# Kernel tuning notes

Measured on AMD Instinct MI355X. Metric: run time of the kernel, lower is better.

Reference implementation:

```python
import jax, jax.numpy as jnp
import numpy as np

B, IN_F, OUT_F = 4096, 4096, 11008  # tokens, in_features, out_features


def setup_inputs() -> dict:
    key = jax.random.key(0)
    k1, k2, k3, k4 = jax.random.split(key, 4)
    x = jax.random.normal(k1, (B, IN_F), dtype=jnp.float32)
    # Each int holds two packed 4-bit codes (low nibble = even col, high nibble = odd col).
    packed_weights = jax.random.randint(k2, (OUT_F, IN_F // 2), 0, 256, dtype=jnp.int32)
    scales = jax.random.uniform(k3, (OUT_F,), dtype=jnp.float32) * 0.02 + 1e-4
    zero_points = jax.random.uniform(k4, (OUT_F,), dtype=jnp.float32) * 15.0
    return {"x": x, "packed_weights": packed_weights, "scales": scales,
            "zero_points": zero_points}


def _dequantize(packed_weights, scales, zero_points):
    # Unpack two 4-bit codes per byte -> q: [OUT_F, IN_F]
    low = (packed_weights & 15).astype(jnp.float32)
    high = ((packed_weights >> 4) & 15).astype(jnp.float32)
    q = jnp.stack([low, high], axis=-1).reshape(packed_weights.shape[0], -1)
    # Per-row affine dequant: w = (q - zero_point) * scale
    return (q - zero_points[:, None]) * scales[:, None]


def reference(x, packed_weights, scales, zero_points):
    W = _dequantize(packed_weights, scales, zero_points)  # [OUT_F, IN_F]
    return x @ W.T  # [B, OUT_F]
```

## Files before the change

### kernel.cpp

```cpp
#include <hip/hip_runtime.h>
#include <hip/hip_bf16.h>
#include <stdint.h>

#define M_DIM 4096
#define N_DIM 11008
#define K_DIM 4096
#define KP    (K_DIM / 2)

typedef __attribute__((ext_vector_type(4))) int i32x4;

#define AS1 __attribute__((address_space(1)))
#define AS3 __attribute__((address_space(3)))

__global__ __launch_bounds__(256) void prep(const float* __restrict__ x,
                                            const int* __restrict__ pw,
                                            signed char* __restrict__ xq,
                                            signed char* __restrict__ wq,
                                            float* __restrict__ r,
                                            float* __restrict__ sx) {
  const int b = blockIdx.x;
  const int t = threadIdx.x;
  if (b < 4096) {
    const int row = b;
    const int lane = t & 63, wid = t >> 6;
    const float4* x4 = (const float4*)(x + (size_t)row * K_DIM);
    float4 v[4];
    float am = 0.0f, sm = 0.0f;
#pragma unroll
    for (int i = 0; i < 4; ++i) {
      v[i] = x4[i * 256 + t];
      sm += v[i].x + v[i].y + v[i].z + v[i].w;
      am = fmaxf(am, fmaxf(fmaxf(fabsf(v[i].x), fabsf(v[i].y)),
                           fmaxf(fabsf(v[i].z), fabsf(v[i].w))));
    }
#pragma unroll
    for (int off = 32; off >= 1; off >>= 1) {
      am = fmaxf(am, __shfl_xor(am, off));
      sm += __shfl_xor(sm, off);
    }
    __shared__ float smax[4], ssum[4];
    if (lane == 0) { smax[wid] = am; ssum[wid] = sm; }
    __syncthreads();
    am = fmaxf(fmaxf(smax[0], smax[1]), fmaxf(smax[2], smax[3]));
    sm = ssum[0] + ssum[1] + ssum[2] + ssum[3];
    const float inv = am > 0.0f ? 127.0f / am : 0.0f;
    unsigned int* xo = (unsigned int*)(xq + (size_t)row * K_DIM);
#pragma unroll
    for (int i = 0; i < 4; ++i) {
      int q0 = min(127, max(-127, __float2int_rn(v[i].x * inv)));
      int q1 = min(127, max(-127, __float2int_rn(v[i].y * inv)));
      int q2 = min(127, max(-127, __float2int_rn(v[i].z * inv)));
      int q3 = min(127, max(-127, __float2int_rn(v[i].w * inv)));
      xo[i * 256 + t] = ((unsigned int)q0 & 0xFF) | (((unsigned int)q1 & 0xFF) << 8) |
                        (((unsigned int)q2 & 0xFF) << 16) | (((unsigned int)q3 & 0xFF) << 24);
    }
    if (t == 0) { r[row] = sm; sx[row] = am > 0.0f ? am / 127.0f : 0.0f; }
  } else {
    const int total = (N_DIM * KP) / 4;
    for (int i = (b - 4096) * 256 + t; i < total; i += 2048 * 256) {
      int4 p = ((const int4*)pw)[i];
      int v[4] = {p.x, p.y, p.z, p.w};
      unsigned int u0 = 0, u1 = 0;
#pragma unroll
      for (int j = 0; j < 2; ++j) {
        unsigned int b0 = (unsigned int)(2 * (v[j] & 15) - 15) & 0xFF;
        unsigned int b1 = (unsigned int)(2 * ((v[j] >> 4) & 15) - 15) & 0xFF;
        u0 |= (b0 | (b1 << 8)) << (16 * j);
      }
#pragma unroll
      for (int j = 0; j < 2; ++j) {
        unsigned int b0 = (unsigned int)(2 * (v[2 + j] & 15) - 15) & 0xFF;
        unsigned int b1 = (unsigned int)(2 * ((v[2 + j] >> 4) & 15) - 15) & 0xFF;
        u1 |= (b0 | (b1 << 8)) << (16 * j);
      }
      uint2 st; st.x = u0; st.y = u1;
      ((uint2*)wq)[i] = st;
    }
  }
}

#define BM 256
#define BN 256
#define BK 128
#define NTILE (K_DIM / BK)
#define NT_M (M_DIM / BM)
#define NT_N (N_DIM / BN)
#define NWG  (NT_M * NT_N)
#define HS 16384
#define PS 65536

#define WAITV(n) asm volatile("s_waitcnt vmcnt(" #n ")" ::: "memory")
#define WAITL0   asm volatile("s_waitcnt lgkmcnt(0)" ::: "memory")
#define BARR     do { asm volatile("" ::: "memory"); __builtin_amdgcn_s_barrier(); asm volatile("" ::: "memory"); } while (0)
#define SCHED0   __builtin_amdgcn_sched_barrier(0)

__global__ __launch_bounds__(512, 2) void gemm_i8(const signed char* __restrict__ Xq,
                                                  const signed char* __restrict__ Wq,
                                                  const float* __restrict__ sc,
                                                  const float* __restrict__ zp,
                                                  const float* __restrict__ rbuf,
                                                  const float* __restrict__ sxbuf,
                                                  float* __restrict__ C) {
  __shared__ __align__(16) unsigned char lds8[131072];

  const int t = threadIdx.x;
  const int bid = blockIdx.x;
  const int swz = (bid & 7) * (NWG / 8) + (bid >> 3);
  const int tm = swz & 15;
  const int tn = swz >> 4;

  const int srow = t >> 3;
  const int g0 = (t & 7) ^ (srow & 7);
  const int koff = g0 * 16;
  const signed char* pB0c0 = Wq + (size_t)(tn * BN + srow) * K_DIM + koff;
  const signed char* pB0c1 = Wq + (size_t)(tn * BN + 64 + srow) * K_DIM + koff;
  const signed char* pB1c0 = Wq + (size_t)(tn * BN + 128 + srow) * K_DIM + koff;
  const signed char* pB1c1 = Wq + (size_t)(tn * BN + 192 + srow) * K_DIM + koff;
  const signed char* pA0c0 = Xq + (size_t)(tm * BM + srow) * K_DIM + koff;
  const signed char* pA0c1 = Xq + (size_t)(tm * BM + 64 + srow) * K_DIM + koff;
  const signed char* pA1c0 = Xq + (size_t)(tm * BM + 128 + srow) * K_DIM + koff;
  const signed char* pA1c1 = Xq + (size_t)(tm * BM + 192 + srow) * K_DIM + koff;
  const int d0 = t * 16;
  const int d1 = d0 + 8192;

  const int lane = t & 63;
  const int w = t >> 6;
  const int wm = w >> 2;
  const int wn = w & 3;
  const int lr = lane & 15, lk = lane >> 4;

  const int j0 = lk ^ (lr & 7);
  const int aB0 = (2 + wm) * HS + lr * 128 + j0 * 16;
  const int aB1 = aB0 ^ 64;
  const int bB0 = (wn >> 1) * HS + (wn & 1) * 8192 + lr * 128 + j0 * 16;
  const int bB1 = bB0 ^ 64;

  i32x4 acc[8][4] = {};

#define GLL(src, dstoff) \
  __builtin_amdgcn_global_load_lds((const AS1 void*)(src), (AS3 void*)(lds8 + (dstoff)), 16, 0, 0)

  GLL(pB0c0, 0 * HS + d0); GLL(pB0c1, 0 * HS + d1);
  GLL(pB1c0, 1 * HS + d0); GLL(pB1c1, 1 * HS + d1);
  GLL(pA0c0, 2 * HS + d0); GLL(pA0c1, 2 * HS + d1);
  GLL(pA1c0, 3 * HS + d0); GLL(pA1c1, 3 * HS + d1);
  GLL(pB0c0 + BK, 4 * HS + d0); GLL(pB0c1 + BK, 4 * HS + d1);
  GLL(pB1c0 + BK, 5 * HS + d0); GLL(pB1c1 + BK, 5 * HS + d1);
  pB0c0 += 2 * BK; pB0c1 += 2 * BK; pB1c0 += 2 * BK; pB1c1 += 2 * BK;
  pA0c0 += BK;     pA0c1 += BK;     pA1c0 += BK;     pA1c1 += BK;
  WAITV(4);
  BARR;

#define TILE(P, SA, SB, VMODE) do {                                                        \
    i32x4 a0[4], a1[4], a2[4], a3[4], b0[4], b1[4];                                        \
                  \
    _Pragma("unroll") for (int i = 0; i < 4; ++i)                                          \
      a0[i] = *(const i32x4*)(lds8 + (P) * PS + aB0 + i * 2048);                           \
    _Pragma("unroll") for (int n = 0; n < 4; ++n)                                          \
      b0[n] = *(const i32x4*)(lds8 + (P) * PS + bB0 + n * 2048);                           \
    _Pragma("unroll") for (int i = 0; i < 4; ++i)                                          \
      a1[i] = *(const i32x4*)(lds8 + (P) * PS + aB0 + (4 + i) * 2048);                     \
    if (SA) { GLL(pA0c0, (((P) ^ 1) * 4 + 2) * HS + d0);                                   \
              GLL(pA0c1, (((P) ^ 1) * 4 + 2) * HS + d1);                                   \
              pA0c0 += BK; pA0c1 += BK; }                                                  \
    SCHED0;                                                                                \
    _Pragma("unroll") for (int i = 0; i < 4; ++i)                                          \
      _Pragma("unroll") for (int n = 0; n < 4; ++n)                                        \
        acc[i][n] = __builtin_amdgcn_mfma_i32_16x16x64_i8(a0[i], b0[n], acc[i][n], 0, 0, 0); \
     \
    _Pragma("unroll") for (int n = 0; n < 4; ++n)                                          \
      b1[n] = *(const i32x4*)(lds8 + (P) * PS + bB1 + n * 2048);                           \
    _Pragma("unroll") for (int i = 0; i < 4; ++i)                                          \
      a2[i] = *(const i32x4*)(lds8 + (P) * PS + aB1 + i * 2048);                           \
    if (SA) { GLL(pA1c0, (((P) ^ 1) * 4 + 3) * HS + d0);                                   \
              GLL(pA1c1, (((P) ^ 1) * 4 + 3) * HS + d1);                                   \
              pA1c0 += BK; pA1c1 += BK; }                                                  \
    SCHED0;                                                                                \
    _Pragma("unroll") for (int i = 0; i < 4; ++i)                                          \
      _Pragma("unroll") for (int n = 0; n < 4; ++n)                                        \
        acc[4 + i][n] = __builtin_amdgcn_mfma_i32_16x16x64_i8(a1[i], b0[n], acc[4 + i][n], 0, 0, 0); \
    WAITL0;                                                                                \
    BARR;                                                                                  \
                            \
    _Pragma("unroll") for (int i = 0; i < 4; ++i)                                          \
      a3[i] = *(const i32x4*)(lds8 + (P) * PS + aB1 + (4 + i) * 2048);                     \
    if (SB) { GLL(pB0c0, ((P) * 4 + 0) * HS + d0);                                         \
              GLL(pB0c1, ((P) * 4 + 0) * HS + d1);                                         \
              pB0c0 += BK; pB0c1 += BK; }                                                  \
    SCHED0;                                                                                \
    _Pragma("unroll") for (int i = 0; i < 4; ++i)                                          \
      _Pragma("unroll") for (int n = 0; n < 4; ++n)                                        \
        acc[i][n] = __builtin_amdgcn_mfma_i32_16x16x64_i8(a2[i], b1[n], acc[i][n], 0, 0, 0); \
                        \
    if (SB) { GLL(pB1c0, ((P) * 4 + 1) * HS + d0);                                         \
              GLL(pB1c1, ((P) * 4 + 1) * HS + d1);                                         \
              pB1c0 += BK; pB1c1 += BK; }                                                  \
    SCHED0;                                                                                \
    _Pragma("unroll") for (int i = 0; i < 4; ++i)                                          \
      _Pragma("unroll") for (int n = 0; n < 4; ++n)                                        \
        acc[4 + i][n] = __builtin_amdgcn_mfma_i32_16x16x64_i8(a3[i], b1[n], acc[4 + i][n], 0, 0, 0); \
    if ((VMODE) == 0) { WAITV(4); } else if ((VMODE) == 1) { WAITV(0); }                   \
    BARR;                                                                                  \
  } while (0)

  for (int it = 0; it < (NTILE - 2) / 2; ++it) {
    TILE(0, 1, 1, 0);
    TILE(1, 1, 1, 0);
  }
  TILE(0, 1, 0, 1);
  TILE(1, 0, 0, 2);

#undef TILE
#undef GLL

  const int row0 = tm * BM + wm * 128 + lk * 4;
  const int col0 = tn * BN + wn * 64 + lr;
  float sv[4], zv[4];
#pragma unroll
  for (int n = 0; n < 4; ++n) {
    sv[n] = sc[col0 + n * 16];
    zv[n] = 7.5f - zp[col0 + n * 16];
  }
#pragma unroll
  for (int m = 0; m < 8; ++m)
#pragma unroll
    for (int rr = 0; rr < 4; ++rr) {
      const int row = row0 + m * 16 + rr;
      const float rv = rbuf[row];
      const float hx = 0.5f * sxbuf[row];
#pragma unroll
      for (int n = 0; n < 4; ++n)
        C[(size_t)row * N_DIM + col0 + n * 16] = sv[n] * (hx * (float)acc[m][n][rr] + zv[n] * rv);
    }
}

__global__ __launch_bounds__(256) void fallback_gemm(const float* __restrict__ x,
                                                     const int* __restrict__ pw,
                                                     const float* __restrict__ sc,
                                                     const float* __restrict__ zp,
                                                     float* __restrict__ out) {
  __shared__ float Xs[64][33];
  __shared__ float Ws[64][33];
  const int bid = blockIdx.x;
  const int bm = bid & 63;
  const int bn = bid >> 6;
  const int t = threadIdx.x;
  const int tx = t & 15, ty = t >> 4;
  float acc[4][4] = {};
  for (int k0 = 0; k0 < K_DIM; k0 += 32) {
    __syncthreads();
#pragma unroll
    for (int i = 0; i < 8; ++i) {
      int e = t + i * 256; int rr = e >> 5, c = e & 31;
      Xs[rr][c] = x[(size_t)(bm * 64 + rr) * K_DIM + k0 + c];
    }
#pragma unroll
    for (int i = 0; i < 4; ++i) {
      int e = t + i * 256; int rr = e >> 4, jj = e & 15;
      int row = bn * 64 + rr;
      int v = pw[(size_t)row * KP + (k0 >> 1) + jj];
      float s = sc[row], z = zp[row];
      Ws[rr][2 * jj]     = ((float)(v & 15) - z) * s;
      Ws[rr][2 * jj + 1] = ((float)((v >> 4) & 15) - z) * s;
    }
    __syncthreads();
#pragma unroll
    for (int kk = 0; kk < 32; ++kk) {
      float a[4], b[4];
#pragma unroll
      for (int i2 = 0; i2 < 4; ++i2) a[i2] = Xs[ty * 4 + i2][kk];
#pragma unroll
      for (int j2 = 0; j2 < 4; ++j2) b[j2] = Ws[tx * 4 + j2][kk];
#pragma unroll
      for (int i2 = 0; i2 < 4; ++i2)
#pragma unroll
        for (int j2 = 0; j2 < 4; ++j2) acc[i2][j2] += a[i2] * b[j2];
    }
  }
#pragma unroll
  for (int i2 = 0; i2 < 4; ++i2)
#pragma unroll
    for (int j2 = 0; j2 < 4; ++j2)
      out[(size_t)(bm * 64 + ty * 4 + i2) * N_DIM + bn * 64 + tx * 4 + j2] = acc[i2][j2];
}

extern "C" void kernel_launch(void* const* d_in, const int* in_sizes, int n_in,
                              void* d_out, int out_size, void* d_ws, size_t ws_size,
                              hipStream_t stream) {
  const float* x  = (const float*)d_in[0];
  const int*   pw = (const int*)d_in[1];
  const float* sc = (const float*)d_in[2];
  const float* zp = (const float*)d_in[3];
  float* out = (float*)d_out;

  const size_t wq_b = (size_t)N_DIM * K_DIM;
  const size_t xq_b = (size_t)M_DIM * K_DIM;
  const size_t need = wq_b + xq_b + 2 * 4096 * sizeof(float);

  if (ws_size >= need) {
    signed char* wq = (signed char*)d_ws;
    signed char* xq = wq + wq_b;
    float* rbuf  = (float*)((char*)d_ws + wq_b + xq_b);
    float* sxbuf = rbuf + 4096;
    hipLaunchKernelGGL(prep,    dim3(4096 + 2048), dim3(256), 0, stream, x, pw, xq, wq, rbuf, sxbuf);
    hipLaunchKernelGGL(gemm_i8, dim3(NWG),         dim3(512), 0, stream, xq, wq, sc, zp, rbuf, sxbuf, out);
  } else {
    hipLaunchKernelGGL(fallback_gemm, dim3(64 * 172), dim3(256), 0, stream, x, pw, sc, zp, out);
  }
}
```

Baseline: 216.8 us.

## Split GEMM workgroup into 16 waves each computing a 64x64 sub-tile

Doubles the workgroup to 1024 threads so each of 16 waves owns a 64x64 output tile instead of 128x64. Accumulator registers are halved and each thread issues one global-to-LDS load per stage instead of two. The pipeline wait counts and the epilogue row mapping are adjusted to match. The aim is more resident waves to hide latency, at the cost of more LDS reads per MFMA and tighter register limits from the new launch bounds.

```diff
diff --git a/kernel.cpp b/kernel.cpp
--- a/kernel.cpp
+++ b/kernel.cpp
@@ -94,13 +94,13 @@
 #define BARR     do { asm volatile("" ::: "memory"); __builtin_amdgcn_s_barrier(); asm volatile("" ::: "memory"); } while (0)
 #define SCHED0   __builtin_amdgcn_sched_barrier(0)
 
-__global__ __launch_bounds__(512, 2) void gemm_i8(const signed char* __restrict__ Xq,
-                                                  const signed char* __restrict__ Wq,
-                                                  const float* __restrict__ sc,
-                                                  const float* __restrict__ zp,
-                                                  const float* __restrict__ rbuf,
-                                                  const float* __restrict__ sxbuf,
-                                                  float* __restrict__ C) {
+__global__ __launch_bounds__(1024, 4) void gemm_i8(const signed char* __restrict__ Xq,
+                                                   const signed char* __restrict__ Wq,
+                                                   const float* __restrict__ sc,
+                                                   const float* __restrict__ zp,
+                                                   const float* __restrict__ rbuf,
+                                                   const float* __restrict__ sxbuf,
+                                                   float* __restrict__ C) {
   __shared__ __align__(16) unsigned char lds8[131072];
 
   const int t = threadIdx.x;
@@ -112,16 +112,11 @@
   const int srow = t >> 3;
   const int g0 = (t & 7) ^ (srow & 7);
   const int koff = g0 * 16;
-  const signed char* pB0c0 = Wq + (size_t)(tn * BN + srow) * K_DIM + koff;
-  const signed char* pB0c1 = Wq + (size_t)(tn * BN + 64 + srow) * K_DIM + koff;
-  const signed char* pB1c0 = Wq + (size_t)(tn * BN + 128 + srow) * K_DIM + koff;
-  const signed char* pB1c1 = Wq + (size_t)(tn * BN + 192 + srow) * K_DIM + koff;
-  const signed char* pA0c0 = Xq + (size_t)(tm * BM + srow) * K_DIM + koff;
-  const signed char* pA0c1 = Xq + (size_t)(tm * BM + 64 + srow) * K_DIM + koff;
-  const signed char* pA1c0 = Xq + (size_t)(tm * BM + 128 + srow) * K_DIM + koff;
-  const signed char* pA1c1 = Xq + (size_t)(tm * BM + 192 + srow) * K_DIM + koff;
-  const int d0 = t * 16;
-  const int d1 = d0 + 8192;
+  const signed char* pB0 = Wq + (size_t)(tn * BN + srow) * K_DIM + koff;
+  const signed char* pB1 = Wq + (size_t)(tn * BN + 128 + srow) * K_DIM + koff;
+  const signed char* pA0 = Xq + (size_t)(tm * BM + srow) * K_DIM + koff;
+  const signed char* pA1 = Xq + (size_t)(tm * BM + 128 + srow) * K_DIM + koff;
+  const int d = t * 16;
 
   const int lane = t & 63;
   const int w = t >> 6;
@@ -130,76 +125,57 @@
   const int lr = lane & 15, lk = lane >> 4;
 
   const int j0 = lk ^ (lr & 7);
-  const int aB0 = (2 + wm) * HS + lr * 128 + j0 * 16;
-  const int aB1 = aB0 ^ 64;
-  const int bB0 = (wn >> 1) * HS + (wn & 1) * 8192 + lr * 128 + j0 * 16;
-  const int bB1 = bB0 ^ 64;
-
-  i32x4 acc[8][4] = {};
+  const int aB0 = (2 + (wm >> 1)) * HS + ((wm & 1) * 64 + lr) * 128 + j0 * 16;
+  const int bB0 = (wn >> 1) * HS + ((wn & 1) * 64 + lr) * 128 + j0 * 16;
+
+  i32x4 acc[4][4] = {};
 
 #define GLL(src, dstoff) \
   __builtin_amdgcn_global_load_lds((const AS1 void*)(src), (AS3 void*)(lds8 + (dstoff)), 16, 0, 0)
 
-  GLL(pB0c0, 0 * HS + d0); GLL(pB0c1, 0 * HS + d1);
-  GLL(pB1c0, 1 * HS + d0); GLL(pB1c1, 1 * HS + d1);
-  GLL(pA0c0, 2 * HS + d0); GLL(pA0c1, 2 * HS + d1);
-  GLL(pA1c0, 3 * HS + d0); GLL(pA1c1, 3 * HS + d1);
-  GLL(pB0c0 + BK, 4 * HS + d0); GLL(pB0c1 + BK, 4 * HS + d1);
-  GLL(pB1c0 + BK, 5 * HS + d0); GLL(pB1c1 + BK, 5 * HS + d1);
-  pB0c0 += 2 * BK; pB0c1 += 2 * BK; pB1c0 += 2 * BK; pB1c1 += 2 * BK;
-  pA0c0 += BK;     pA0c1 += BK;     pA1c0 += BK;     pA1c1 += BK;
-  WAITV(4);
+  GLL(pB0, 0 * HS + d);
+  GLL(pB1, 1 * HS + d);
+  GLL(pA0, 2 * HS + d);
+  GLL(pA1, 3 * HS + d);
+  GLL(pB0 + BK, 4 * HS + d);
+  GLL(pB1 + BK, 5 * HS + d);
+  pB0 += 2 * BK; pB1 += 2 * BK;
+  pA0 += BK;     pA1 += BK;
+  WAITV(2);
   BARR;
 
 #define TILE(P, SA, SB, VMODE) do {                                                        \
-    i32x4 a0[4], a1[4], a2[4], a3[4], b0[4], b1[4];                                        \
-                  \
+    i32x4 a0[4], b0[4], a1[4], b1[4];                                                      \
+                            \
     _Pragma("unroll") for (int i = 0; i < 4; ++i)                                          \
       a0[i] = *(const i32x4*)(lds8 + (P) * PS + aB0 + i * 2048);                           \
     _Pragma("unroll") for (int n = 0; n < 4; ++n)                                          \
       b0[n] = *(const i32x4*)(lds8 + (P) * PS + bB0 + n * 2048);                           \
-    _Pragma("unroll") for (int i = 0; i < 4; ++i)                                          \
-      a1[i] = *(const i32x4*)(lds8 + (P) * PS + aB0 + (4 + i) * 2048);                     \
-    if (SA) { GLL(pA0c0, (((P) ^ 1) * 4 + 2) * HS + d0);                                   \
-              GLL(pA0c1, (((P) ^ 1) * 4 + 2) * HS + d1);                                   \
-              pA0c0 += BK; pA0c1 += BK; }                                                  \
+    if (SA) { GLL(pA0, (((P) ^ 1) * 4 + 2) * HS + d); pA0 += BK; }                         \
     SCHED0;                                                                                \
     _Pragma("unroll") for (int i = 0; i < 4; ++i)                                          \
       _Pragma("unroll") for (int n = 0; n < 4; ++n)                                        \
         acc[i][n] = __builtin_amdgcn_mfma_i32_16x16x64_i8(a0[i], b0[n], acc[i][n], 0, 0, 0); \
      \
+    _Pragma("unroll") for (int i = 0; i < 4; ++i)                                          \
+      a1[i] = *(const i32x4*)(lds8 + (P) * PS + (aB0 ^ 64) + i * 2048);                    \
     _Pragma("unroll") for (int n = 0; n < 4; ++n)                                          \
-      b1[n] = *(const i32x4*)(lds8 + (P) * PS + bB1 + n * 2048);                           \
-    _Pragma("unroll") for (int i = 0; i < 4; ++i)                                          \
-      a2[i] = *(const i32x4*)(lds8 + (P) * PS + aB1 + i * 2048);                           \
-    if (SA) { GLL(pA1c0, (((P) ^ 1) * 4 + 3) * HS + d0);                                   \
-              GLL(pA1c1, (((P) ^ 1) * 4 + 3) * HS + d1);                                   \
-              pA1c0 += BK; pA1c1 += BK; }                                                  \
+      b1[n] = *(const i32x4*)(lds8 + (P) * PS + (bB0 ^ 64) + n * 2048);                    \
+    if (SA) { GLL(pA1, (((P) ^ 1) * 4 + 3) * HS + d); pA1 += BK; }                         \
     SCHED0;                                                                                \
     _Pragma("unroll") for (int i = 0; i < 4; ++i)                                          \
-      _Pragma("unroll") for (int n = 0; n < 4; ++n)                                        \
-        acc[4 + i][n] = __builtin_amdgcn_mfma_i32_16x16x64_i8(a1[i], b0[n], acc[4 + i][n], 0, 0, 0); \
+      _Pragma("unroll") for (int n = 0; n < 2; ++n)                                        \
+        acc[i][n] = __builtin_amdgcn_mfma_i32_16x16x64_i8(a1[i], b1[n], acc[i][n], 0, 0, 0); \
     WAITL0;                                                                                \
     BARR;                                                                                  \
-                            \
-    _Pragma("unroll") for (int i = 0; i < 4; ++i)                                          \
-      a3[i] = *(const i32x4*)(lds8 + (P) * PS + aB1 + (4 + i) * 2048);                     \
-    if (SB) { GLL(pB0c0, ((P) * 4 + 0) * HS + d0);                                         \
-              GLL(pB0c1, ((P) * 4 + 0) * HS + d1);                                         \
-              pB0c0 += BK; pB0c1 += BK; }                                                  \
+                 \
+    if (SB) { GLL(pB0, ((P) * 4 + 0) * HS + d); pB0 += BK;                                 \
+              GLL(pB1, ((P) * 4 + 1) * HS + d); pB1 += BK; }                               \
     SCHED0;                                                                                \
     _Pragma("unroll") for (int i = 0; i < 4; ++i)                                          \
-      _Pragma("unroll") for (int n = 0; n < 4; ++n)                                        \
-        acc[i][n] = __builtin_amdgcn_mfma_i32_16x16x64_i8(a2[i], b1[n], acc[i][n], 0, 0, 0); \
-                        \
-    if (SB) { GLL(pB1c0, ((P) * 4 + 1) * HS + d0);                                         \
-              GLL(pB1c1, ((P) * 4 + 1) * HS + d1);                                         \
-              pB1c0 += BK; pB1c1 += BK; }                                                  \
-    SCHED0;                                                                                \
-    _Pragma("unroll") for (int i = 0; i < 4; ++i)                                          \
-      _Pragma("unroll") for (int n = 0; n < 4; ++n)                                        \
-        acc[4 + i][n] = __builtin_amdgcn_mfma_i32_16x16x64_i8(a3[i], b1[n], acc[4 + i][n], 0, 0, 0); \
-    if ((VMODE) == 0) { WAITV(4); } else if ((VMODE) == 1) { WAITV(0); }                   \
+      _Pragma("unroll") for (int n = 2; n < 4; ++n)                                        \
+        acc[i][n] = __builtin_amdgcn_mfma_i32_16x16x64_i8(a1[i], b1[n], acc[i][n], 0, 0, 0); \
+    if ((VMODE) == 0) { WAITV(2); } else if ((VMODE) == 1) { WAITV(0); }                   \
     BARR;                                                                                  \
   } while (0)
 
@@ -213,7 +189,7 @@
 #undef TILE
 #undef GLL
 
-  const int row0 = tm * BM + wm * 128 + lk * 4;
+  const int row0 = tm * BM + wm * 64 + lk * 4;
   const int col0 = tn * BN + wn * 64 + lr;
   float sv[4], zv[4];
 #pragma unroll
@@ -222,15 +198,15 @@
     zv[n] = 7.5f - zp[col0 + n * 16];
   }
 #pragma unroll
-  for (int m = 0; m < 8; ++m)
+  for (int i = 0; i < 4; ++i)
 #pragma unroll
     for (int rr = 0; rr < 4; ++rr) {
-      const int row = row0 + m * 16 + rr;
+      const int row = row0 + i * 16 + rr;
       const float rv = rbuf[row];
       const float hx = 0.5f * sxbuf[row];
 #pragma unroll
       for (int n = 0; n < 4; ++n)
-        C[(size_t)row * N_DIM + col0 + n * 16] = sv[n] * (hx * (float)acc[m][n][rr] + zv[n] * rv);
+        C[(size_t)row * N_DIM + col0 + n * 16] = sv[n] * (hx * (float)acc[i][n][rr] + zv[n] * rv);
     }
 }
 
@@ -302,8 +278,8 @@
     signed char* xq = wq + wq_b;
     float* rbuf  = (float*)((char*)d_ws + wq_b + xq_b);
     float* sxbuf = rbuf + 4096;
-    hipLaunchKernelGGL(prep,    dim3(4096 + 2048), dim3(256), 0, stream, x, pw, xq, wq, rbuf, sxbuf);
-    hipLaunchKernelGGL(gemm_i8, dim3(NWG),         dim3(512), 0, stream, xq, wq, sc, zp, rbuf, sxbuf, out);
+    hipLaunchKernelGGL(prep,    dim3(4096 + 2048), dim3(256),  0, stream, x, pw, xq, wq, rbuf, sxbuf);
+    hipLaunchKernelGGL(gemm_i8, dim3(NWG),         dim3(1024), 0, stream, xq, wq, sc, zp, rbuf, sxbuf, out);
   } else {
     hipLaunchKernelGGL(fallback_gemm, dim3(64 * 172), dim3(256), 0, stream, x, pw, sc, zp, out);
   }
```

Measured after the change: 272.0 us. +25.5%, slower.

## Load B weights directly from global into registers, halve LDS footprint

Applied to the files above, without the earlier changes.

The weight (B) operand no longer goes through LDS. Each wave loads its B fragments straight from global memory into registers, double-buffered across tiles, and only the activation (A) tiles are staged in LDS with a 2-stage buffer. LDS use drops from 128KB to 64KB and the mid-tile barrier and LDS wait go away. In exchange, each wave issues uncoalesced 16-byte global loads for B with a vmcnt(0) wait every tile, so global latency may be exposed and B data is re-fetched redundantly across waves that share columns.

```diff
diff --git a/kernel.cpp b/kernel.cpp
--- a/kernel.cpp
+++ b/kernel.cpp
@@ -87,10 +87,9 @@
 #define NT_N (N_DIM / BN)
 #define NWG  (NT_M * NT_N)
 #define HS 16384
-#define PS 65536
+#define PS 32768
 
 #define WAITV(n) asm volatile("s_waitcnt vmcnt(" #n ")" ::: "memory")
-#define WAITL0   asm volatile("s_waitcnt lgkmcnt(0)" ::: "memory")
 #define BARR     do { asm volatile("" ::: "memory"); __builtin_amdgcn_s_barrier(); asm volatile("" ::: "memory"); } while (0)
 #define SCHED0   __builtin_amdgcn_sched_barrier(0)
 
@@ -101,7 +100,7 @@
                                                   const float* __restrict__ rbuf,
                                                   const float* __restrict__ sxbuf,
                                                   float* __restrict__ C) {
-  __shared__ __align__(16) unsigned char lds8[131072];
+  __shared__ __align__(16) unsigned char lds8[65536];
 
   const int t = threadIdx.x;
   const int bid = blockIdx.x;
@@ -112,10 +111,6 @@
   const int srow = t >> 3;
   const int g0 = (t & 7) ^ (srow & 7);
   const int koff = g0 * 16;
-  const signed char* pB0c0 = Wq + (size_t)(tn * BN + srow) * K_DIM + koff;
-  const signed char* pB0c1 = Wq + (size_t)(tn * BN + 64 + srow) * K_DIM + koff;
-  const signed char* pB1c0 = Wq + (size_t)(tn * BN + 128 + srow) * K_DIM + koff;
-  const signed char* pB1c1 = Wq + (size_t)(tn * BN + 192 + srow) * K_DIM + koff;
   const signed char* pA0c0 = Xq + (size_t)(tm * BM + srow) * K_DIM + koff;
   const signed char* pA0c1 = Xq + (size_t)(tm * BM + 64 + srow) * K_DIM + koff;
   const signed char* pA1c0 = Xq + (size_t)(tm * BM + 128 + srow) * K_DIM + koff;
@@ -130,85 +125,72 @@
   const int lr = lane & 15, lk = lane >> 4;
 
   const int j0 = lk ^ (lr & 7);
-  const int aB0 = (2 + wm) * HS + lr * 128 + j0 * 16;
-  const int aB1 = aB0 ^ 64;
-  const int bB0 = (wn >> 1) * HS + (wn & 1) * 8192 + lr * 128 + j0 * 16;
-  const int bB1 = bB0 ^ 64;
+  const int aP0 = wm * HS + lr * 128 + j0 * 16;
+
+  const signed char* pBl = Wq + (size_t)(tn * BN + (wn >> 1) * 128 + (wn & 1) * 64 + lr) * K_DIM + lk * 16;
 
   i32x4 acc[8][4] = {};
+  i32x4 bA[4], bB[4], bc1[4];
 
 #define GLL(src, dstoff) \
   __builtin_amdgcn_global_load_lds((const AS1 void*)(src), (AS3 void*)(lds8 + (dstoff)), 16, 0, 0)
 
-  GLL(pB0c0, 0 * HS + d0); GLL(pB0c1, 0 * HS + d1);
-  GLL(pB1c0, 1 * HS + d0); GLL(pB1c1, 1 * HS + d1);
-  GLL(pA0c0, 2 * HS + d0); GLL(pA0c1, 2 * HS + d1);
-  GLL(pA1c0, 3 * HS + d0); GLL(pA1c1, 3 * HS + d1);
-  GLL(pB0c0 + BK, 4 * HS + d0); GLL(pB0c1 + BK, 4 * HS + d1);
-  GLL(pB1c0 + BK, 5 * HS + d0); GLL(pB1c1 + BK, 5 * HS + d1);
-  pB0c0 += 2 * BK; pB0c1 += 2 * BK; pB1c0 += 2 * BK; pB1c1 += 2 * BK;
-  pA0c0 += BK;     pA0c1 += BK;     pA1c0 += BK;     pA1c1 += BK;
-  WAITV(4);
+#pragma unroll
+  for (int n = 0; n < 4; ++n)
+    bA[n] = *(const i32x4*)(pBl + (size_t)n * 16 * K_DIM);
+  GLL(pA0c0, d0); GLL(pA0c1, d1);
+  GLL(pA1c0, HS + d0); GLL(pA1c1, HS + d1);
+  pA0c0 += BK; pA0c1 += BK; pA1c0 += BK; pA1c1 += BK;
+  WAITV(0);
   BARR;
 
-#define TILE(P, SA, SB, VMODE) do {                                                        \
-    i32x4 a0[4], a1[4], a2[4], a3[4], b0[4], b1[4];                                        \
-                  \
-    _Pragma("unroll") for (int i = 0; i < 4; ++i)                                          \
-      a0[i] = *(const i32x4*)(lds8 + (P) * PS + aB0 + i * 2048);                           \
+#define TILE(P, BC, BN_, SA, SB, WEND) do {                                                \
+    i32x4 a[4];                                                                            \
+      \
     _Pragma("unroll") for (int n = 0; n < 4; ++n)                                          \
-      b0[n] = *(const i32x4*)(lds8 + (P) * PS + bB0 + n * 2048);                           \
-    _Pragma("unroll") for (int i = 0; i < 4; ++i)                                          \
-      a1[i] = *(const i32x4*)(lds8 + (P) * PS + aB0 + (4 + i) * 2048);                     \
-    if (SA) { GLL(pA0c0, (((P) ^ 1) * 4 + 2) * HS + d0);                                   \
-              GLL(pA0c1, (((P) ^ 1) * 4 + 2) * HS + d1);                                   \
-              pA0c0 += BK; pA0c1 += BK; }                                                  \
-    SCHED0;                                                                                \
-    _Pragma("unroll") for (int i = 0; i < 4; ++i)                                          \
-      _Pragma("unroll") for (int n = 0; n < 4; ++n)                                        \
-        acc[i][n] = __builtin_amdgcn_mfma_i32_16x16x64_i8(a0[i], b0[n], acc[i][n], 0, 0, 0); \
-     \
-    _Pragma("unroll") for (int n = 0; n < 4; ++n)                                          \
-      b1[n] = *(const i32x4*)(lds8 + (P) * PS + bB1 + n * 2048);                           \
-    _Pragma("unroll") for (int i = 0; i < 4; ++i)                                          \
-      a2[i] = *(const i32x4*)(lds8 + (P) * PS + aB1 + i * 2048);                           \
-    if (SA) { GLL(pA1c0, (((P) ^ 1) * 4 + 3) * HS + d0);                                   \
-              GLL(pA1c1, (((P) ^ 1) * 4 + 3) * HS + d1);                                   \
-              pA1c0 += BK; pA1c1 += BK; }                                                  \
-    SCHED0;                                                                                \
-    _Pragma("unroll") for (int i = 0; i < 4; ++i)                                          \
-      _Pragma("unroll") for (int n = 0; n < 4; ++n)                                        \
-        acc[4 + i][n] = __builtin_amdgcn_mfma_i32_16x16x64_i8(a1[i], b0[n], acc[4 + i][n], 0, 0, 0); \
-    WAITL0;                                                                                \
-    BARR;                                                                                  \
-                            \
-    _Pragma("unroll") for (int i = 0; i < 4; ++i)                                          \
-      a3[i] = *(const i32x4*)(lds8 + (P) * PS + aB1 + (4 + i) * 2048);                     \
-    if (SB) { GLL(pB0c0, ((P) * 4 + 0) * HS + d0);                                         \
-              GLL(pB0c1, ((P) * 4 + 0) * HS + d1);                                         \
-              pB0c0 += BK; pB0c1 += BK; }                                                  \
-    SCHED0;                                                                                \
-    _Pragma("unroll") for (int i = 0; i < 4; ++i)                                          \
-      _Pragma("unroll") for (int n = 0; n < 4; ++n)                                        \
-        acc[i][n] = __builtin_amdgcn_mfma_i32_16x16x64_i8(a2[i], b1[n], acc[i][n], 0, 0, 0); \
-                        \
-    if (SB) { GLL(pB1c0, ((P) * 4 + 1) * HS + d0);                                         \
-              GLL(pB1c1, ((P) * 4 + 1) * HS + d1);                                         \
-              pB1c0 += BK; pB1c1 += BK; }                                                  \
-    SCHED0;                                                                                \
-    _Pragma("unroll") for (int i = 0; i < 4; ++i)                                          \
-      _Pragma("unroll") for (int n = 0; n < 4; ++n)                                        \
-        acc[4 + i][n] = __builtin_amdgcn_mfma_i32_16x16x64_i8(a3[i], b1[n], acc[4 + i][n], 0, 0, 0); \
-    if ((VMODE) == 0) { WAITV(4); } else if ((VMODE) == 1) { WAITV(0); }                   \
-    BARR;                                                                                  \
+      bc1[n] = *(const i32x4*)(pBl + 64 + (size_t)n * 16 * K_DIM);                         \
+    if (SB) { _Pragma("unroll") for (int n = 0; n < 4; ++n)                                \
+      BN_[n] = *(const i32x4*)(pBl + BK + (size_t)n * 16 * K_DIM); }                       \
+    if (SA) { GLL(pA0c0, ((P) ^ 1) * PS + d0); GLL(pA0c1, ((P) ^ 1) * PS + d1);            \
+              GLL(pA1c0, ((P) ^ 1) * PS + HS + d0); GLL(pA1c1, ((P) ^ 1) * PS + HS + d1);  \
+              pA0c0 += BK; pA0c1 += BK; pA1c0 += BK; pA1c1 += BK; }                        \
+    _Pragma("unroll") for (int i = 0; i < 4; ++i)                                          \
+      a[i] = *(const i32x4*)(lds8 + (P) * PS + aP0 + i * 2048);                            \
+    SCHED0;                                                                                \
+    _Pragma("unroll") for (int i = 0; i < 4; ++i)                                          \
+      _Pragma("unroll") for (int n = 0; n < 4; ++n)                                        \
+        acc[i][n] = __builtin_amdgcn_mfma_i32_16x16x64_i8(a[i], BC[n], acc[i][n], 0, 0, 0); \
+                                                  \
+    _Pragma("unroll") for (int i = 0; i < 4; ++i)                                          \
+      a[i] = *(const i32x4*)(lds8 + (P) * PS + aP0 + (4 + i) * 2048);                      \
+    SCHED0;                                                                                \
+    _Pragma("unroll") for (int i = 0; i < 4; ++i)                                          \
+      _Pragma("unroll") for (int n = 0; n < 4; ++n)                                        \
+        acc[4 + i][n] = __builtin_amdgcn_mfma_i32_16x16x64_i8(a[i], BC[n], acc[4 + i][n], 0, 0, 0); \
+                      \
+    _Pragma("unroll") for (int i = 0; i < 4; ++i)                                          \
+      a[i] = *(const i32x4*)(lds8 + (P) * PS + (aP0 ^ 64) + i * 2048);                     \
+    SCHED0;                                                                                \
+    _Pragma("unroll") for (int i = 0; i < 4; ++i)                                          \
+      _Pragma("unroll") for (int n = 0; n < 4; ++n)                                        \
+        acc[i][n] = __builtin_amdgcn_mfma_i32_16x16x64_i8(a[i], bc1[n], acc[i][n], 0, 0, 0); \
+                                 \
+    _Pragma("unroll") for (int i = 0; i < 4; ++i)                                          \
+      a[i] = *(const i32x4*)(lds8 + (P) * PS + (aP0 ^ 64) + (4 + i) * 2048);               \
+    SCHED0;                                                                                \
+    _Pragma("unroll") for (int i = 0; i < 4; ++i)                                          \
+      _Pragma("unroll") for (int n = 0; n < 4; ++n)                                        \
+        acc[4 + i][n] = __builtin_amdgcn_mfma_i32_16x16x64_i8(a[i], bc1[n], acc[4 + i][n], 0, 0, 0); \
+    pBl += BK;                                                                             \
+    if (WEND) { WAITV(0); BARR; }                                                          \
   } while (0)
 
-  for (int it = 0; it < (NTILE - 2) / 2; ++it) {
-    TILE(0, 1, 1, 0);
-    TILE(1, 1, 1, 0);
-  }
-  TILE(0, 1, 0, 1);
-  TILE(1, 0, 0, 2);
+  for (int it = 0; it < 15; ++it) {
+    TILE(0, bA, bB, 1, 1, 1);
+    TILE(1, bB, bA, 1, 1, 1);
+  }
+  TILE(0, bA, bB, 1, 1, 1);
+  TILE(1, bB, bA, 0, 0, 0);
 
 #undef TILE
 #undef GLL
```

After: 324.6 us. 49.7% more time.
